# Kernel tuning notes

Measured on AMD Instinct MI355X. Metric: run time of the kernel, lower is better.

Reference implementation:

```python
import jax, jax.numpy as jnp
import numpy as np

PUNISH_COEF = -100.0
BIG_NEG = 1e10


def setup_inputs() -> dict:
    key = jax.random.key(0)
    k1, k2, k3, k4, k5, k6, k7 = jax.random.split(key, 7)
    N, A, E = 500_000, 5, 2_000_000
    logits = jax.random.normal(k1, (N, A), dtype=jnp.float32)
    illegal_action_masks = (jax.random.uniform(k2, (N, A)) < 0.1).astype(jnp.float32)
    # conflict_pairs columns: [agent1, act1, agent2, act2, mask]
    agent1 = jax.random.randint(k3, (E,), 0, N)
    act1 = jax.random.randint(k4, (E,), 0, A)
    agent2 = jax.random.randint(k5, (E,), 0, N)
    act2 = jax.random.randint(k6, (E,), 0, A)
    mask = jax.random.randint(k7, (E,), 0, 2)
    conflict_pairs = jnp.stack([agent1, act1, agent2, act2, mask], axis=1).astype(jnp.int64)
    return {
        "logits": logits,
        "illegal_action_masks": illegal_action_masks,
        "conflict_pairs": conflict_pairs,
        "iterations": 10,
    }


def reference(logits, illegal_action_masks, conflict_pairs, iterations):
    N, A = logits.shape
    agent1 = conflict_pairs[:, 0]
    act1 = conflict_pairs[:, 1]
    agent2 = conflict_pairs[:, 2]
    act2 = conflict_pairs[:, 3]
    masks = conflict_pairs[:, 4].astype(logits.dtype)
    index1 = agent1 * A + act1  # scatter destination (flat over N*A)
    index2 = agent2 * A + act2  # gather source (flat over N*A)
    illegal_penalty = BIG_NEG * illegal_action_masks

    q_logits = jnp.zeros_like(logits) - illegal_penalty
    for _ in range(iterations):
        q_probs = jax.nn.softmax(q_logits, axis=-1).reshape(-1)  # (N*A,)
        contrib = q_probs[index2] * masks  # (E,)
        punishments = jax.ops.segment_sum(contrib, index1, num_segments=N * A) * PUNISH_COEF
        q_logits = logits + punishments.reshape(N, A) - illegal_penalty
    return q_logits
```

## Files before the change

### kernel.cpp

```cpp
#include <hip/hip_runtime.h>
#include <hip/hip_bf16.h>

static constexpr int ACT = 5;
static constexpr float PUNISH = -100.0f;
static constexpr float BIGNEG = 1.0e10f;
static constexpr int ITERS = 10;
static constexpr float QSCALE = 255.0f;
static constexpr float PUNISH_Q = PUNISH / 255.0f;
#define BLK 256
#define PBLK 512
#define SCAN_T 1024
#define W 1280
#define CHUNK 8192
#define MAXNB 2048
#define CS_B 16
#define CS_R 32

__device__ __forceinline__ int xcd_swz(int bid, int G) {
    int q = G >> 3, r = G & 7;
    int xcd = bid & 7, idx = bid >> 3;
    return (xcd < r ? xcd * (q + 1) : r * (q + 1) + (xcd - r) * q) + idx;
}

__global__ void k_packhist2(const int* __restrict__ pairs, int E, int nb,
                            int2* __restrict__ packedA, unsigned char* __restrict__ wcnt,
                            int* __restrict__ bh1, int* __restrict__ bh2) {
    __shared__ int h1[MAXNB];
    __shared__ int h2[MAXNB];
    for (int k = threadIdx.x; k < nb; k += PBLK) { h1[k] = 0; h2[k] = 0; }
    __syncthreads();
    int base = blockIdx.x * CHUNK;
    int lane = threadIdx.x & 63;
#pragma unroll 4
    for (int j = 0; j < CHUNK / PBLK; j++) {
        int t = base + j * PBLK + threadIdx.x;
        bool live = false;
        int i1 = 0, i2 = 0, m = 0;
        if (t < E) {
            const int* r = pairs + 5 * t;
            m = r[4];
            if (m != 0) {
                live = true;
                i1 = r[0] * ACT + r[1];
                i2 = r[2] * ACT + r[3];
            }
        }
        unsigned long long b = __ballot(live);
        if (live) {
            int prefix = __popcll(b & ((1ull << lane) - 1));
            packedA[(t & ~63) + prefix] = make_int2(i1 | (m << 24), i2);
            atomicAdd(&h1[i1 / W], 1);
            atomicAdd(&h2[i2 / W], 1);
        }
        if (lane == 0 && t < E) wcnt[t >> 6] = (unsigned char)__popcll(b);
    }
    __syncthreads();
    size_t off = (size_t)blockIdx.x * nb;
    for (int k = threadIdx.x; k < nb; k += PBLK) { bh1[off + k] = h1[k]; bh2[off + k] = h2[k]; }
}

__global__ void k_colscan2(const int* __restrict__ bhA, int* __restrict__ bhOffA, int* __restrict__ ttA,
                           const int* __restrict__ bhB, int* __restrict__ bhOffB, int* __restrict__ ttB,
                           int G, int nb) {
    const int* bh    = (blockIdx.y == 0) ? bhA : bhB;
    int* bhOff       = (blockIdx.y == 0) ? bhOffA : bhOffB;
    int* tt          = (blockIdx.y == 0) ? ttA : ttB;
    __shared__ int part[CS_R][CS_B];
    int c = threadIdx.x % CS_B;
    int r = threadIdx.x / CS_B;
    int j = blockIdx.x * CS_B + c;
    int per = (G + CS_R - 1) / CS_R;
    int g0 = r * per, g1 = min(g0 + per, G);
    int s = 0;
    if (j < nb)
        for (int g = g0; g < g1; g++) s += bh[(size_t)g * nb + j];
    part[r][c] = s;
    __syncthreads();
    int run = 0;
    for (int u = 0; u < r; u++) run += part[u][c];
    if (j < nb) {
        if (r == CS_R - 1) tt[j] = run + s;
        for (int g = g0; g < g1; g++) {
            int v = bh[(size_t)g * nb + j];
            bhOff[(size_t)g * nb + j] = run;
            run += v;
        }
    }
}

__global__ void k_scan2(const int* __restrict__ cnt1, int* __restrict__ pos1,
                        const int* __restrict__ cnt2, int* __restrict__ pos2, int nb) {
    __shared__ int sums[SCAN_T];
    int tid = threadIdx.x;
    int L = (nb + SCAN_T - 1) / SCAN_T;
    int lo = tid * L, hi = min(lo + L, nb);
#pragma unroll
    for (int which = 0; which < 2; which++) {
        const int* cnt = (which == 0) ? cnt1 : cnt2;
        int* pos       = (which == 0) ? pos1 : pos2;
        int s = 0;
        for (int i = lo; i < hi; i++) s += cnt[i];
        sums[tid] = s;
        __syncthreads();
        for (int off = 1; off < SCAN_T; off <<= 1) {
            int add = (tid >= off) ? sums[tid - off] : 0;
            __syncthreads();
            sums[tid] += add;
            __syncthreads();
        }
        int run = sums[tid] - s;
        for (int i = lo; i < hi; i++) {
            int c = cnt[i];
            pos[i] = run;
            run += c;
        }
        if (tid == SCAN_T - 1) pos[nb] = sums[SCAN_T - 1];
        __syncthreads();
    }
}

__global__ void k_reorder2(const int2* __restrict__ packedA, const unsigned char* __restrict__ wcnt,
                           int E, int nb, int G,
                           const int* __restrict__ bhOff1, const int* __restrict__ pos1,
                           const int* __restrict__ bhOff2, const int* __restrict__ pos2,
                           unsigned int* __restrict__ centry, unsigned short* __restrict__ pentry) {
    __shared__ int h1[MAXNB];
    __shared__ int h2[MAXNB];
    __shared__ int lb1[MAXNB];
    __shared__ int lb2[MAXNB];
    int row = xcd_swz(blockIdx.x, G);
    size_t hoff = (size_t)row * nb;
    for (int k = threadIdx.x; k < nb; k += PBLK) {
        h1[k] = 0; h2[k] = 0;
        lb1[k] = pos1[k] + bhOff1[hoff + k];
        lb2[k] = pos2[k] + bhOff2[hoff + k];
    }
    __syncthreads();
    int base = row * CHUNK;
#pragma unroll 4
    for (int j = 0; j < CHUNK / PBLK; j++) {
        int t = base + j * PBLK + threadIdx.x;
        if (t < E && (t & 63) < (int)wcnt[t >> 6]) {
            int2 e = packedA[t];
            int i1 = e.x & 0xFFFFFF;
            int m  = (e.x >> 24) & 0xFF;
            int i2 = e.y;
            int bk1 = i1 / W;
            int bk2 = i2 / W;
            int r1 = atomicAdd(&h1[bk1], 1);
            int r2 = atomicAdd(&h2[bk2], 1);
            int p1 = lb1[bk1] + r1;
            int p2 = lb2[bk2] + r2;
            centry[p1] = ((unsigned int)(i1 - bk1 * W) << 21) | (unsigned int)p2;
            pentry[p2] = (unsigned short)(((i2 - bk2 * W) << 5) | (m & 31));
        }
    }
}

__global__ void __launch_bounds__(BLK, 8)
k_firstC(const float* __restrict__ lg, const float* __restrict__ il,
         __hip_bfloat16* __restrict__ adjbf,
         const unsigned short* __restrict__ pentry, const int* __restrict__ pos2,
         unsigned char* __restrict__ contrib, int na) {
    __shared__ float win[W];
    int j = blockIdx.x;
    int base = j * W;
    int lim = min(W, na - base);
    int o = threadIdx.x * 5;
    if (o < lim) {
        float q0[5], p0[5];
#pragma unroll
        for (int a = 0; a < 5; a++) {
            float l = lg[base + o + a];
            float i = il[base + o + a];
            adjbf[base + o + a] = __float2bfloat16(fmaf(-BIGNEG, i, l));
            q0[a] = -BIGNEG * i;
        }
        float mx = q0[0];
#pragma unroll
        for (int a = 1; a < 5; a++) mx = fmaxf(mx, q0[a]);
        float ssum = 0.f;
#pragma unroll
        for (int a = 0; a < 5; a++) { p0[a] = __expf(q0[a] - mx); ssum += p0[a]; }
        float inv = 1.0f / ssum;
#pragma unroll
        for (int a = 0; a < 5; a++) win[o + a] = p0[a] * inv;
    }
    __syncthreads();
    int p0i = pos2[j], p1i = pos2[j + 1];
    for (int k = p0i + threadIdx.x; k < p1i; k += BLK) {
        unsigned int v = pentry[k];
        float val = fminf(win[v >> 5] * (float)(v & 31) * QSCALE, 255.0f);
        contrib[k] = (unsigned char)__float2uint_rn(val);
    }
}

__global__ void __launch_bounds__(BLK, 8)
k_iterC(const unsigned int* __restrict__ centry, const int* __restrict__ pos1,
        const unsigned char* __restrict__ cOld, unsigned char* __restrict__ cNew,
        const unsigned short* __restrict__ pentry, const int* __restrict__ pos2,
        const __hip_bfloat16* __restrict__ adjbf, float* __restrict__ out,
        int last, int na) {
    __shared__ int win[W];
    int j = blockIdx.x;
    int base = j * W;
    int lim = min(W, na - base);
    int4 z = make_int4(0, 0, 0, 0);
    for (int k = threadIdx.x; k < W / 4; k += BLK) ((int4*)win)[k] = z;
    __syncthreads();
    int c0 = pos1[j], c1 = pos1[j + 1];
    for (int t = c0 + threadIdx.x; t < c1; t += BLK) {
        unsigned int u = centry[t];
        atomicAdd(&win[u >> 21], (int)cOld[u & 0x1FFFFF]);
    }
    __syncthreads();
    int o = threadIdx.x * 5;
    if (o < lim) {
        float q[5];
#pragma unroll
        for (int a = 0; a < 5; a++)
            q[a] = fmaf(PUNISH_Q, (float)win[o + a], __bfloat162float(adjbf[base + o + a]));
        if (last) {
#pragma unroll
            for (int a = 0; a < 5; a++) out[base + o + a] = q[a];
        } else {
            float mx = q[0];
#pragma unroll
            for (int a = 1; a < 5; a++) mx = fmaxf(mx, q[a]);
            float ssum = 0.f, p[5];
#pragma unroll
            for (int a = 0; a < 5; a++) { p[a] = __expf(q[a] - mx); ssum += p[a]; }
            float inv = 1.0f / ssum;
#pragma unroll
            for (int a = 0; a < 5; a++) win[o + a] = __float_as_int(p[a] * inv);
        }
    }
    if (!last) {
        __syncthreads();
        int p0i = pos2[j], p1i = pos2[j + 1];
        for (int k = p0i + threadIdx.x; k < p1i; k += BLK) {
            unsigned int v = pentry[k];
            float val = fminf(__int_as_float(win[v >> 5]) * (float)(v & 31) * QSCALE, 255.0f);
            cNew[k] = (unsigned char)__float2uint_rn(val);
        }
    }
}

__global__ void k_softmax_first_sc(const float* __restrict__ illegal,
                                   float* __restrict__ probs, float* __restrict__ s, int n) {
    int i = blockIdx.x * BLK + threadIdx.x;
    if (i >= n) return;
    int base = i * ACT;
    float q[5], p[5];
#pragma unroll
    for (int a = 0; a < 5; a++) q[a] = -BIGNEG * illegal[base + a];
    float mx = q[0];
#pragma unroll
    for (int a = 1; a < 5; a++) mx = fmaxf(mx, q[a]);
    float ssum = 0.f;
#pragma unroll
    for (int a = 0; a < 5; a++) { p[a] = __expf(q[a] - mx); ssum += p[a]; }
    float inv = 1.0f / ssum;
#pragma unroll
    for (int a = 0; a < 5; a++) { probs[base + a] = p[a] * inv; s[base + a] = 0.f; }
}

__global__ void k_softmax_step_sc(const float* __restrict__ logits,
                                  const float* __restrict__ illegal,
                                  float* __restrict__ s,
                                  float* __restrict__ probs, int n) {
    int i = blockIdx.x * BLK + threadIdx.x;
    if (i >= n) return;
    int base = i * ACT;
    float q[5], p[5];
#pragma unroll
    for (int a = 0; a < 5; a++) {
        float adj = fmaf(-BIGNEG, illegal[base + a], logits[base + a]);
        q[a] = fmaf(PUNISH, s[base + a], adj);
    }
    float mx = q[0];
#pragma unroll
    for (int a = 1; a < 5; a++) mx = fmaxf(mx, q[a]);
    float ssum = 0.f;
#pragma unroll
    for (int a = 0; a < 5; a++) { p[a] = __expf(q[a] - mx); ssum += p[a]; }
    float inv = 1.0f / ssum;
#pragma unroll
    for (int a = 0; a < 5; a++) { probs[base + a] = p[a] * inv; s[base + a] = 0.f; }
}

__global__ void k_scatter_raw(const int* __restrict__ pairs, int E,
                              const float* __restrict__ probs, float* __restrict__ s) {
    int t = blockIdx.x * BLK + threadIdx.x;
    if (t >= E) return;
    const int* r = pairs + 5 * t;
    int m = r[4];
    if (m == 0) return;
    unsafeAtomicAdd(&s[r[0] * ACT + r[1]], probs[r[2] * ACT + r[3]] * (float)m);
}

__global__ void k_final_sc(const float* __restrict__ logits,
                           const float* __restrict__ illegal,
                           const float* __restrict__ s,
                           float* __restrict__ out, int na) {
    int i = blockIdx.x * BLK + threadIdx.x;
    if (i >= na) return;
    float adj = fmaf(-BIGNEG, illegal[i], logits[i]);
    out[i] = fmaf(PUNISH, s[i], adj);
}

extern "C" void kernel_launch(void* const* d_in, const int* in_sizes, int n_in,
                              void* d_out, int out_size, void* d_ws, size_t ws_size,
                              hipStream_t stream) {
    const float* logits  = (const float*)d_in[0];
    const float* illegal = (const float*)d_in[1];
    const int*   pairs   = (const int*)d_in[2];
    float* out = (float*)d_out;

    const int na = in_sizes[0];
    const int n  = na / ACT;
    const int E  = in_sizes[2] / 5;
    const int nw = (E + 63) / 64;
    const int nb = (na + W - 1) / W;
    const int G  = (E + CHUNK - 1) / CHUNK;

    auto cdiv = [](int a, int b) { return (a + b - 1) / b; };

    size_t off = 0;
    auto alloc = [&](size_t bytes) { size_t o = off; off = (off + bytes + 15) & ~(size_t)15; return o; };
    size_t o_abf = alloc((size_t)na * 2);
    size_t o_cA  = alloc((size_t)E);
    size_t o_cB  = alloc((size_t)E);
    size_t o_pA  = alloc((size_t)E * 8);
    size_t o_ce  = alloc((size_t)E * 4);
    size_t o_pe  = alloc((size_t)E * 2);
    size_t o_bh1 = alloc((size_t)G * nb * 4);
    size_t o_bO1 = alloc((size_t)G * nb * 4);
    size_t o_bh2 = alloc((size_t)G * nb * 4);
    size_t o_bO2 = alloc((size_t)G * nb * 4);
    size_t o_tt1 = alloc((size_t)nb * 4);
    size_t o_tt2 = alloc((size_t)nb * 4);
    size_t o_po1 = alloc((size_t)(nb + 1) * 4);
    size_t o_po2 = alloc((size_t)(nb + 1) * 4);
    size_t o_wc  = alloc((size_t)nw);
    const size_t need = off;

    char* w = (char*)d_ws;

    if (na % 20 == 0 && nb <= MAXNB && E <= (1 << 21) && ws_size >= need) {
        __hip_bfloat16* adjbf = (__hip_bfloat16*)(w + o_abf);
        unsigned char* cA = (unsigned char*)(w + o_cA);
        unsigned char* cB = (unsigned char*)(w + o_cB);
        int2* pA = (int2*)(w + o_pA);
        unsigned int*   ce = (unsigned int*)(w + o_ce);
        unsigned short* pe = (unsigned short*)(w + o_pe);
        int* bh1 = (int*)(w + o_bh1);
        int* bO1 = (int*)(w + o_bO1);
        int* bh2 = (int*)(w + o_bh2);
        int* bO2 = (int*)(w + o_bO2);
        int* tt1 = (int*)(w + o_tt1);
        int* tt2 = (int*)(w + o_tt2);
        int* po1 = (int*)(w + o_po1);
        int* po2 = (int*)(w + o_po2);
        unsigned char* wc = (unsigned char*)(w + o_wc);

        k_packhist2<<<G, PBLK, 0, stream>>>(pairs, E, nb, pA, wc, bh1, bh2);
        k_colscan2<<<dim3(cdiv(nb, CS_B), 2), CS_B * CS_R, 0, stream>>>(
            bh1, bO1, tt1, bh2, bO2, tt2, G, nb);
        k_scan2<<<1, SCAN_T, 0, stream>>>(tt1, po1, tt2, po2, nb);
        k_reorder2<<<G, PBLK, 0, stream>>>(pA, wc, E, nb, G,
                                           bO1, po1, bO2, po2, ce, pe);

        k_firstC<<<nb, BLK, 0, stream>>>(logits, illegal, adjbf, pe, po2, cA, na);

        for (int t = 1; t <= ITERS; t++) {
            unsigned char* src = (t & 1) ? cA : cB;
            unsigned char* dst = (t & 1) ? cB : cA;
            k_iterC<<<nb, BLK, 0, stream>>>(ce, po1, src, dst, pe, po2, adjbf, out,
                                            (t == ITERS) ? 1 : 0, na);
        }
    } else {
        float* s = (float*)d_ws;
        float* probs = out;
        for (int t = 1; t <= ITERS; t++) {
            if (t == 1)
                k_softmax_first_sc<<<cdiv(n, BLK), BLK, 0, stream>>>(illegal, probs, s, n);
            else
                k_softmax_step_sc<<<cdiv(n, BLK), BLK, 0, stream>>>(logits, illegal, s, probs, n);
            k_scatter_raw<<<cdiv(E, BLK), BLK, 0, stream>>>(pairs, E, probs, s);
        }
        k_final_sc<<<cdiv(na, BLK), BLK, 0, stream>>>(logits, illegal, s, out, na);
    }
}
```

Before: 140.2 us.

## Replace push-side contribution buffer with direct gather from quantized per-action probs

Drops the second bucketing pass over gather indices, so each iteration no longer writes per-edge contributions. Instead it writes quantized 8-bit probabilities per action (na bytes) and gathers them randomly by flat index in the scatter loop, multiplied by a per-edge mask byte. Window width shrinks from 1280 to 1020, which raises the bucket count and grows MAXNB to fit the 22-bit index field. This cuts preprocessing work and per-iteration edge-sized writes, at the cost of random global gathers over a 2.5 MB byte array instead of sequential reads.

```diff
diff --git a/kernel.cpp b/kernel.cpp
--- a/kernel.cpp
+++ b/kernel.cpp
@@ -10,9 +10,9 @@
 #define BLK 256
 #define PBLK 512
 #define SCAN_T 1024
-#define W 1280
+#define W 1020
 #define CHUNK 8192
-#define MAXNB 2048
+#define MAXNB 2560
 #define CS_B 16
 #define CS_R 32
 
@@ -22,12 +22,11 @@
     return (xcd < r ? xcd * (q + 1) : r * (q + 1) + (xcd - r) * q) + idx;
 }
 
-__global__ void k_packhist2(const int* __restrict__ pairs, int E, int nb,
+__global__ void k_packhist1(const int* __restrict__ pairs, int E, int nb,
                             int2* __restrict__ packedA, unsigned char* __restrict__ wcnt,
-                            int* __restrict__ bh1, int* __restrict__ bh2) {
+                            int* __restrict__ bh1) {
     __shared__ int h1[MAXNB];
-    __shared__ int h2[MAXNB];
-    for (int k = threadIdx.x; k < nb; k += PBLK) { h1[k] = 0; h2[k] = 0; }
+    for (int k = threadIdx.x; k < nb; k += PBLK) h1[k] = 0;
     __syncthreads();
     int base = blockIdx.x * CHUNK;
     int lane = threadIdx.x & 63;
@@ -50,21 +49,16 @@
             int prefix = __popcll(b & ((1ull << lane) - 1));
             packedA[(t & ~63) + prefix] = make_int2(i1 | (m << 24), i2);
             atomicAdd(&h1[i1 / W], 1);
-            atomicAdd(&h2[i2 / W], 1);
         }
         if (lane == 0 && t < E) wcnt[t >> 6] = (unsigned char)__popcll(b);
     }
     __syncthreads();
     size_t off = (size_t)blockIdx.x * nb;
-    for (int k = threadIdx.x; k < nb; k += PBLK) { bh1[off + k] = h1[k]; bh2[off + k] = h2[k]; }
-}
-
-__global__ void k_colscan2(const int* __restrict__ bhA, int* __restrict__ bhOffA, int* __restrict__ ttA,
-                           const int* __restrict__ bhB, int* __restrict__ bhOffB, int* __restrict__ ttB,
-                           int G, int nb) {
-    const int* bh    = (blockIdx.y == 0) ? bhA : bhB;
-    int* bhOff       = (blockIdx.y == 0) ? bhOffA : bhOffB;
-    int* tt          = (blockIdx.y == 0) ? ttA : ttB;
+    for (int k = threadIdx.x; k < nb; k += PBLK) bh1[off + k] = h1[k];
+}
+
+__global__ void k_colscan1(const int* __restrict__ bh, int* __restrict__ bhOff,
+                           int* __restrict__ tt, int G, int nb) {
     __shared__ int part[CS_R][CS_B];
     int c = threadIdx.x % CS_B;
     int r = threadIdx.x / CS_B;
@@ -88,52 +82,41 @@
     }
 }
 
-__global__ void k_scan2(const int* __restrict__ cnt1, int* __restrict__ pos1,
-                        const int* __restrict__ cnt2, int* __restrict__ pos2, int nb) {
+__global__ void k_scan1(const int* __restrict__ cnt, int* __restrict__ pos, int nb) {
     __shared__ int sums[SCAN_T];
     int tid = threadIdx.x;
     int L = (nb + SCAN_T - 1) / SCAN_T;
     int lo = tid * L, hi = min(lo + L, nb);
-#pragma unroll
-    for (int which = 0; which < 2; which++) {
-        const int* cnt = (which == 0) ? cnt1 : cnt2;
-        int* pos       = (which == 0) ? pos1 : pos2;
-        int s = 0;
-        for (int i = lo; i < hi; i++) s += cnt[i];
-        sums[tid] = s;
+    int s = 0;
+    for (int i = lo; i < hi; i++) s += cnt[i];
+    sums[tid] = s;
+    __syncthreads();
+    for (int off = 1; off < SCAN_T; off <<= 1) {
+        int add = (tid >= off) ? sums[tid - off] : 0;
         __syncthreads();
-        for (int off = 1; off < SCAN_T; off <<= 1) {
-            int add = (tid >= off) ? sums[tid - off] : 0;
-            __syncthreads();
-            sums[tid] += add;
-            __syncthreads();
-        }
-        int run = sums[tid] - s;
-        for (int i = lo; i < hi; i++) {
-            int c = cnt[i];
-            pos[i] = run;
-            run += c;
-        }
-        if (tid == SCAN_T - 1) pos[nb] = sums[SCAN_T - 1];
+        sums[tid] += add;
         __syncthreads();
     }
-}
-
-__global__ void k_reorder2(const int2* __restrict__ packedA, const unsigned char* __restrict__ wcnt,
+    int run = sums[tid] - s;
+    for (int i = lo; i < hi; i++) {
+        int c = cnt[i];
+        pos[i] = run;
+        run += c;
+    }
+    if (tid == SCAN_T - 1) pos[nb] = sums[SCAN_T - 1];
+}
+
+__global__ void k_reorder1(const int2* __restrict__ packedA, const unsigned char* __restrict__ wcnt,
                            int E, int nb, int G,
                            const int* __restrict__ bhOff1, const int* __restrict__ pos1,
-                           const int* __restrict__ bhOff2, const int* __restrict__ pos2,
-                           unsigned int* __restrict__ centry, unsigned short* __restrict__ pentry) {
+                           unsigned int* __restrict__ centry, unsigned char* __restrict__ cm) {
     __shared__ int h1[MAXNB];
-    __shared__ int h2[MAXNB];
     __shared__ int lb1[MAXNB];
-    __shared__ int lb2[MAXNB];
     int row = xcd_swz(blockIdx.x, G);
     size_t hoff = (size_t)row * nb;
     for (int k = threadIdx.x; k < nb; k += PBLK) {
-        h1[k] = 0; h2[k] = 0;
+        h1[k] = 0;
         lb1[k] = pos1[k] + bhOff1[hoff + k];
-        lb2[k] = pos2[k] + bhOff2[hoff + k];
     }
     __syncthreads();
     int base = row * CHUNK;
@@ -146,23 +129,17 @@
             int m  = (e.x >> 24) & 0xFF;
             int i2 = e.y;
             int bk1 = i1 / W;
-            int bk2 = i2 / W;
             int r1 = atomicAdd(&h1[bk1], 1);
-            int r2 = atomicAdd(&h2[bk2], 1);
             int p1 = lb1[bk1] + r1;
-            int p2 = lb2[bk2] + r2;
-            centry[p1] = ((unsigned int)(i1 - bk1 * W) << 21) | (unsigned int)p2;
-            pentry[p2] = (unsigned short)(((i2 - bk2 * W) << 5) | (m & 31));
+            centry[p1] = ((unsigned int)(i1 - bk1 * W) << 22) | (unsigned int)i2;
+            cm[p1] = (unsigned char)m;
         }
     }
 }
 
 __global__ void __launch_bounds__(BLK, 8)
 k_firstC(const float* __restrict__ lg, const float* __restrict__ il,
-         __hip_bfloat16* __restrict__ adjbf,
-         const unsigned short* __restrict__ pentry, const int* __restrict__ pos2,
-         unsigned char* __restrict__ contrib, int na) {
-    __shared__ float win[W];
+         __hip_bfloat16* __restrict__ adjbf, unsigned char* __restrict__ probs, int na) {
     int j = blockIdx.x;
     int base = j * W;
     int lim = min(W, na - base);
@@ -182,23 +159,17 @@
         float ssum = 0.f;
 #pragma unroll
         for (int a = 0; a < 5; a++) { p0[a] = __expf(q0[a] - mx); ssum += p0[a]; }
-        float inv = 1.0f / ssum;
-#pragma unroll
-        for (int a = 0; a < 5; a++) win[o + a] = p0[a] * inv;
-    }
-    __syncthreads();
-    int p0i = pos2[j], p1i = pos2[j + 1];
-    for (int k = p0i + threadIdx.x; k < p1i; k += BLK) {
-        unsigned int v = pentry[k];
-        float val = fminf(win[v >> 5] * (float)(v & 31) * QSCALE, 255.0f);
-        contrib[k] = (unsigned char)__float2uint_rn(val);
+        float inv = QSCALE / ssum;
+#pragma unroll
+        for (int a = 0; a < 5; a++)
+            probs[base + o + a] = (unsigned char)__float2uint_rn(p0[a] * inv);
     }
 }
 
 __global__ void __launch_bounds__(BLK, 8)
-k_iterC(const unsigned int* __restrict__ centry, const int* __restrict__ pos1,
-        const unsigned char* __restrict__ cOld, unsigned char* __restrict__ cNew,
-        const unsigned short* __restrict__ pentry, const int* __restrict__ pos2,
+k_iterC(const unsigned int* __restrict__ centry, const unsigned char* __restrict__ cm,
+        const int* __restrict__ pos1,
+        const unsigned char* __restrict__ pOld, unsigned char* __restrict__ pNew,
         const __hip_bfloat16* __restrict__ adjbf, float* __restrict__ out,
         int last, int na) {
     __shared__ int win[W];
@@ -211,7 +182,8 @@
     int c0 = pos1[j], c1 = pos1[j + 1];
     for (int t = c0 + threadIdx.x; t < c1; t += BLK) {
         unsigned int u = centry[t];
-        atomicAdd(&win[u >> 21], (int)cOld[u & 0x1FFFFF]);
+        int val = (int)pOld[u & 0x3FFFFF] * (int)cm[t];
+        atomicAdd(&win[u >> 22], val);
     }
     __syncthreads();
     int o = threadIdx.x * 5;
@@ -230,18 +202,10 @@
             float ssum = 0.f, p[5];
 #pragma unroll
             for (int a = 0; a < 5; a++) { p[a] = __expf(q[a] - mx); ssum += p[a]; }
-            float inv = 1.0f / ssum;
-#pragma unroll
-            for (int a = 0; a < 5; a++) win[o + a] = __float_as_int(p[a] * inv);
-        }
-    }
-    if (!last) {
-        __syncthreads();
-        int p0i = pos2[j], p1i = pos2[j + 1];
-        for (int k = p0i + threadIdx.x; k < p1i; k += BLK) {
-            unsigned int v = pentry[k];
-            float val = fminf(__int_as_float(win[v >> 5]) * (float)(v & 31) * QSCALE, 255.0f);
-            cNew[k] = (unsigned char)__float2uint_rn(val);
+            float inv = QSCALE / ssum;
+#pragma unroll
+            for (int a = 0; a < 5; a++)
+                pNew[base + o + a] = (unsigned char)__float2uint_rn(p[a] * inv);
         }
     }
 }
@@ -329,54 +293,43 @@
     size_t off = 0;
     auto alloc = [&](size_t bytes) { size_t o = off; off = (off + bytes + 15) & ~(size_t)15; return o; };
     size_t o_abf = alloc((size_t)na * 2);
-    size_t o_cA  = alloc((size_t)E);
-    size_t o_cB  = alloc((size_t)E);
-    size_t o_pA  = alloc((size_t)E * 8);
+    size_t o_pA8 = alloc((size_t)na);
+    size_t o_pB8 = alloc((size_t)na);
+    size_t o_pk  = alloc((size_t)E * 8);
     size_t o_ce  = alloc((size_t)E * 4);
-    size_t o_pe  = alloc((size_t)E * 2);
+    size_t o_cm  = alloc((size_t)E);
     size_t o_bh1 = alloc((size_t)G * nb * 4);
     size_t o_bO1 = alloc((size_t)G * nb * 4);
-    size_t o_bh2 = alloc((size_t)G * nb * 4);
-    size_t o_bO2 = alloc((size_t)G * nb * 4);
     size_t o_tt1 = alloc((size_t)nb * 4);
-    size_t o_tt2 = alloc((size_t)nb * 4);
     size_t o_po1 = alloc((size_t)(nb + 1) * 4);
-    size_t o_po2 = alloc((size_t)(nb + 1) * 4);
     size_t o_wc  = alloc((size_t)nw);
     const size_t need = off;
 
     char* w = (char*)d_ws;
 
-    if (na % 20 == 0 && nb <= MAXNB && E <= (1 << 21) && ws_size >= need) {
+    if (na % 20 == 0 && nb <= MAXNB && na <= (1 << 22) && ws_size >= need) {
         __hip_bfloat16* adjbf = (__hip_bfloat16*)(w + o_abf);
-        unsigned char* cA = (unsigned char*)(w + o_cA);
-        unsigned char* cB = (unsigned char*)(w + o_cB);
-        int2* pA = (int2*)(w + o_pA);
-        unsigned int*   ce = (unsigned int*)(w + o_ce);
-        unsigned short* pe = (unsigned short*)(w + o_pe);
+        unsigned char* p8[2] = {(unsigned char*)(w + o_pA8), (unsigned char*)(w + o_pB8)};
+        int2* pA = (int2*)(w + o_pk);
+        unsigned int*  ce = (unsigned int*)(w + o_ce);
+        unsigned char* cm = (unsigned char*)(w + o_cm);
         int* bh1 = (int*)(w + o_bh1);
         int* bO1 = (int*)(w + o_bO1);
-        int* bh2 = (int*)(w + o_bh2);
-        int* bO2 = (int*)(w + o_bO2);
         int* tt1 = (int*)(w + o_tt1);
-        int* tt2 = (int*)(w + o_tt2);
         int* po1 = (int*)(w + o_po1);
-        int* po2 = (int*)(w + o_po2);
         unsigned char* wc = (unsigned char*)(w + o_wc);
 
-        k_packhist2<<<G, PBLK, 0, stream>>>(pairs, E, nb, pA, wc, bh1, bh2);
-        k_colscan2<<<dim3(cdiv(nb, CS_B), 2), CS_B * CS_R, 0, stream>>>(
-            bh1, bO1, tt1, bh2, bO2, tt2, G, nb);
-        k_scan2<<<1, SCAN_T, 0, stream>>>(tt1, po1, tt2, po2, nb);
-        k_reorder2<<<G, PBLK, 0, stream>>>(pA, wc, E, nb, G,
-                                           bO1, po1, bO2, po2, ce, pe);
-
-        k_firstC<<<nb, BLK, 0, stream>>>(logits, illegal, adjbf, pe, po2, cA, na);
+        k_packhist1<<<G, PBLK, 0, stream>>>(pairs, E, nb, pA, wc, bh1);
+        k_colscan1<<<cdiv(nb, CS_B), CS_B * CS_R, 0, stream>>>(bh1, bO1, tt1, G, nb);
+        k_scan1<<<1, SCAN_T, 0, stream>>>(tt1, po1, nb);
+        k_reorder1<<<G, PBLK, 0, stream>>>(pA, wc, E, nb, G, bO1, po1, ce, cm);
+
+        k_firstC<<<nb, BLK, 0, stream>>>(logits, illegal, adjbf, p8[0], na);
 
         for (int t = 1; t <= ITERS; t++) {
-            unsigned char* src = (t & 1) ? cA : cB;
-            unsigned char* dst = (t & 1) ? cB : cA;
-            k_iterC<<<nb, BLK, 0, stream>>>(ce, po1, src, dst, pe, po2, adjbf, out,
+            unsigned char* src = p8[(t - 1) & 1];
+            unsigned char* dst = p8[t & 1];
+            k_iterC<<<nb, BLK, 0, stream>>>(ce, cm, po1, src, dst, adjbf, out,
                                             (t == ITERS) ? 1 : 0, na);
         }
     } else {
```

Measured after the change: 157.4 us. 1.12x slower.
